# Kernel optimization log

Measured on AMD Instinct MI355X. Metric: run time of the kernel, lower is better.

## Reference

```python
import jax, jax.numpy as jnp
import numpy as np

B, L, D = 2, 4096, 2048
H = 8
DK = D // H   # head qk dim = 256
DV = D // H   # head v dim = 256
KCONV = 4
BT = 64       # chunk size
EPS = 1e-5


def setup_inputs() -> dict:
    key = jax.random.key(0)
    ks = jax.random.split(key, 10)
    s = 0.02  # xavier-ish init scale (gain 2**-2.5)
    return {
        "hidden_states": jax.random.normal(ks[0], (B, L, D), jnp.float32),
        "Wq": jax.random.normal(ks[1], (D, D), jnp.float32) * s,
        "Wk": jax.random.normal(ks[2], (D, D), jnp.float32) * s,
        "Wv": jax.random.normal(ks[3], (D, D), jnp.float32) * s,
        "Wb": jax.random.normal(ks[4], (H, D), jnp.float32) * s,
        "conv_q": jax.random.normal(ks[5], (D, KCONV), jnp.float32) * 0.5,
        "conv_k": jax.random.normal(ks[6], (D, KCONV), jnp.float32) * 0.5,
        "conv_v": jax.random.normal(ks[7], (D, KCONV), jnp.float32) * 0.5,
        "g_norm": jnp.ones((DV,), jnp.float32),
        "Wo": jax.random.normal(ks[8], (D, D), jnp.float32) * s,
    }


def _causal_conv_silu(x, w):
    # depthwise causal conv1d (ShortConvolution), x: [B,L,C], w: [C,K]; silu activation
    K = w.shape[1]
    xp = jnp.pad(x, ((0, 0), (K - 1, 0), (0, 0)))
    Lx = x.shape[1]
    y = xp[:, 0:Lx, :] * w[:, 0]
    for j in range(1, K):
        y = y + xp[:, j:j + Lx, :] * w[:, j]
    return jax.nn.silu(y)


def _l2norm(x):
    return x * jax.lax.rsqrt(jnp.sum(x * x, -1, keepdims=True) + 1e-6)


def _chunk_delta_rule(q, k, v, beta):
    # q,k: [B,H,L,DK], v: [B,H,L,DV], beta: [B,H,L]
    b, h, Lq, dk = q.shape
    dv = v.shape[-1]
    nc = Lq // BT
    q = q * (dk ** -0.5)
    kb = k * beta[..., None]
    vb = v * beta[..., None]
    ch = lambda x: x.reshape(b, h, nc, BT, x.shape[-1])
    qc, kc, kbc, vbc = ch(q), ch(k), ch(kb), ch(vb)
    tri_s = jnp.tril(jnp.ones((BT, BT), bool), -1)  # strictly lower
    tri = jnp.tril(jnp.ones((BT, BT), bool))        # lower incl diag
    # M = strict_lower(K_beta K^T); T = (I+M)^{-1} via unit-lower triangular solve
    M = jnp.where(tri_s, jnp.einsum('bhntd,bhnsd->bhnts', kbc, kc), 0.0)
    Lmat = jnp.eye(BT, dtype=q.dtype) + M
    W = jax.scipy.linalg.solve_triangular(Lmat, kbc, lower=True, unit_diagonal=True)  # T @ k_beta
    U = jax.scipy.linalg.solve_triangular(Lmat, vbc, lower=True, unit_diagonal=True)  # T @ v_beta

    def step(S, xs):
        q_i, k_i, w_i, u_i = xs  # each [b,h,BT,d]
        attn = jnp.where(tri, jnp.einsum('bhtd,bhsd->bhts', q_i, k_i), 0.0)
        u_new = u_i - jnp.einsum('bhtd,bhdv->bhtv', w_i, S)
        o_i = jnp.einsum('bhtd,bhdv->bhtv', q_i, S) + jnp.einsum('bhts,bhsv->bhtv', attn, u_new)
        S = S + jnp.einsum('bhtd,bhtv->bhdv', k_i, u_new)
        return S, o_i

    mv = lambda x: jnp.moveaxis(x, 2, 0)  # chunk axis to front for scan
    S0 = jnp.zeros((b, h, dk, dv), q.dtype)
    S, o = jax.lax.scan(step, S0, (mv(qc), mv(kc), mv(W), mv(U)))
    o = jnp.moveaxis(o, 0, 2).reshape(b, h, Lq, dv)
    return o, S


def reference(hidden_states, Wq, Wk, Wv, Wb, conv_q, conv_k, conv_v, g_norm, Wo):
    hs = hidden_states
    q = _causal_conv_silu(hs @ Wq.T, conv_q)
    k = _causal_conv_silu(hs @ Wk.T, conv_k)
    v = _causal_conv_silu(hs @ Wv.T, conv_v)
    tohead = lambda x: x.reshape(B, L, H, -1).transpose(0, 2, 1, 3)  # b l (h d) -> b h l d
    q, k, v = tohead(q), tohead(k), tohead(v)
    q, k = _l2norm(q), _l2norm(k)
    beta = jax.nn.sigmoid(hs @ Wb.T).transpose(0, 2, 1)  # [B,H,L]
    o, _ = _chunk_delta_rule(q, k, v, beta)
    o = o.transpose(0, 2, 1, 3)  # [B,L,H,DV]
    o = o * jax.lax.rsqrt(jnp.mean(o * o, -1, keepdims=True) + EPS) * g_norm  # per-head RMSNorm
    return o.reshape(B, L, D) @ Wo.T
```

## Files before the change

### kernel.cpp

```cpp
#include <hip/hip_runtime.h>
#include <stdint.h>

#define TOK    8192
#define LDIM   4096
#define DDIM   2048
#define NBH    16
#define DK     256
#define NCHUNK 64

typedef __attribute__((ext_vector_type(8))) short bf16x8;
typedef __attribute__((ext_vector_type(4))) float f32x4;

#define MFMA(a,b,c) __builtin_amdgcn_mfma_f32_16x16x32_bf16((a),(b),(c),0,0,0)

__device__ __forceinline__ unsigned short f2bf(float f){
  union { float f; uint32_t u; } v; v.f = f;
  uint32_t r = v.u + 0x7FFFu + ((v.u >> 16) & 1u);
  return (unsigned short)(r >> 16);
}
__device__ __forceinline__ float bf2f(unsigned short u){
  union { uint32_t u; float f; } v; v.u = ((uint32_t)u) << 16;
  return v.f;
}

typedef __attribute__((address_space(1))) unsigned int as1_u32;
typedef __attribute__((address_space(3))) unsigned int as3_u32;
__device__ __forceinline__ void gload16(const void* g, void* l){
  __builtin_amdgcn_global_load_lds((const as1_u32*)g, (as3_u32*)l, 16, 0, 0);
}

__global__ void k_guard(float* o){ if (threadIdx.x == 0) o[0] = 0.f; }

__global__ __launch_bounds__(256) void k_f2bf(const float* __restrict__ s,
                                              unsigned short* __restrict__ d, int n)
{
  int i = (blockIdx.x*256 + threadIdx.x)*4;
  if (i >= n) return;
  float4 v = *(const float4*)(s + i);
  ushort4 o; o.x=f2bf(v.x); o.y=f2bf(v.y); o.z=f2bf(v.z); o.w=f2bf(v.w);
  *(ushort4*)(d + i) = o;
}

__global__ __launch_bounds__(256) void k_beta(const float* __restrict__ hs,
                                              const float* __restrict__ Wb,
                                              float* __restrict__ beta)
{
  const long t = blockIdx.x;
  const int tid = threadIdx.x;
  float acc[8] = {0,0,0,0,0,0,0,0};
  const float* xr = hs + t*DDIM;
  for (int i = tid; i < DDIM; i += 256){
    float x = xr[i];
    #pragma unroll
    for (int h=0; h<8; h++) acc[h] += x * Wb[h*DDIM + i];
  }
  __shared__ float red[8][4];
  const int w = tid >> 6, lane = tid & 63;
  #pragma unroll
  for (int h=0; h<8; h++){
    float s = acc[h];
    #pragma unroll
    for (int off=32; off; off>>=1) s += __shfl_down(s, off, 64);
    if (lane == 0) red[h][w] = s;
  }
  __syncthreads();
  if (tid < 8){
    float s = red[tid][0]+red[tid][1]+red[tid][2]+red[tid][3];
    float bv = 1.f/(1.f + __expf(-s));
    int b = (int)(t >> 12), l = (int)(t & 4095);
    beta[((long)(b*8 + tid))*LDIM + l] = bv;
  }
}

template <bool F32OUT>
__global__ __launch_bounds__(256,2) void k_gemm_bt(
    const unsigned short* __restrict__ A, const unsigned short* __restrict__ Bw,
    void* __restrict__ Cv, int M, int N, int K)
{
  __shared__ unsigned short As[128*32];
  __shared__ unsigned short Bs[128*32];
  const int tid = threadIdx.x;
  const int w = tid >> 6, l = tid & 63;
  const int lo = l & 15, quad = l >> 4;
  const int wm = w >> 1, wn = w & 1;
  const int gx = gridDim.x;
  int id = blockIdx.y * gx + blockIdx.x;
  const int nwg = gx * gridDim.y;
  if ((nwg & 7) == 0){
    const int q8 = nwg >> 3;
    id = (id & 7) * q8 + (id >> 3);
  }
  const int bx = id % gx, by = id / gx;
  const long tm = (long)by * 128, tn = (long)bx * 128;
  const int slot0 = (w*2+0)*64 + l;
  const int slot1 = (w*2+1)*64 + l;
  const int r0 = slot0 >> 2, c0 = (slot0 & 3) * 8;
  const int r1 = slot1 >> 2, c1 = (slot1 & 3) * 8;
  const unsigned short* pA0 = A  + (tm + r0)*(long)K + c0;
  const unsigned short* pA1 = A  + (tm + r1)*(long)K + c1;
  const unsigned short* pB0 = Bw + (tn + r0)*(long)K + c0;
  const unsigned short* pB1 = Bw + (tn + r1)*(long)K + c1;
  unsigned short* lA0 = &As[slot0*8]; unsigned short* lA1 = &As[slot1*8];
  unsigned short* lB0 = &Bs[slot0*8]; unsigned short* lB1 = &Bs[slot1*8];
  f32x4 acc[4][4] = {};
  for (int k0 = 0; k0 < K; k0 += 32){
    __syncthreads();
    gload16(pA0 + k0, lA0);
    gload16(pA1 + k0, lA1);
    gload16(pB0 + k0, lB0);
    gload16(pB1 + k0, lB1);
    __syncthreads();
    bf16x8 af[4], bg[4];
    #pragma unroll
    for (int i=0;i<4;i++){
      af[i] = *(const bf16x8*)&As[(wm*64 + i*16 + lo)*32 + quad*8];
      bg[i] = *(const bf16x8*)&Bs[(wn*64 + i*16 + lo)*32 + quad*8];
    }
    #pragma unroll
    for (int mt=0; mt<4; mt++)
      #pragma unroll
      for (int nt=0; nt<4; nt++)
        acc[mt][nt] = MFMA(af[mt], bg[nt], acc[mt][nt]);
  }
  #pragma unroll
  for (int mt=0; mt<4; mt++)
    #pragma unroll
    for (int nt=0; nt<4; nt++)
      #pragma unroll
      for (int r=0; r<4; r++){
        long m = tm + wm*64 + mt*16 + quad*4 + r;
        long n = tn + wn*64 + nt*16 + lo;
        if (F32OUT) ((float*)Cv)[m*N + n] = acc[mt][nt][r];
        else ((unsigned short*)Cv)[m*N + n] = f2bf(acc[mt][nt][r]);
      }
}

__global__ __launch_bounds__(256) void k_conv(
  const unsigned short* __restrict__ X, const float* __restrict__ Wc,
  const float* __restrict__ beta,
  unsigned short* __restrict__ O, int mode)
{
  const int lt = blockIdx.x, bh = blockIdx.y;
  const int b = bh >> 3, h = bh & 7;
  const int d = threadIdx.x;
  const int ch = h*256 + d;
  const int l0 = lt*64;
  const unsigned short* xp = X + (long)b*LDIM*DDIM + ch;
  const float4 wv = *(const float4*)(Wc + ch*4);
  float x0=0.f, x1=0.f, x2=0.f;
  if (l0 >= 3){
    x0 = bf2f(xp[(long)(l0-3)*DDIM]);
    x1 = bf2f(xp[(long)(l0-2)*DDIM]);
    x2 = bf2f(xp[(long)(l0-1)*DDIM]);
  }
  float y[64];
  #pragma unroll
  for (int i=0;i<64;i++){
    float x3 = bf2f(xp[(long)(l0+i)*DDIM]);
    float s = x0*wv.x + x1*wv.y + x2*wv.z + x3*wv.w;
    y[i] = s / (1.f + __expf(-s));
    x0 = x1; x1 = x2; x2 = x3;
  }
  unsigned short* op = O + (long)bh*LDIM*DK + d;
  if (mode == 2){
    const float* bet = beta + (long)bh*LDIM + l0;
    #pragma unroll
    for (int i=0;i<64;i++) op[(long)(l0+i)*DK] = f2bf(y[i]*bet[i]);
    return;
  }
  __shared__ float red[64*4];
  __shared__ float scl[64];
  const int wv_i = threadIdx.x >> 6, lane = threadIdx.x & 63;
  #pragma unroll
  for (int i=0;i<64;i++){
    float ss = y[i]*y[i];
    #pragma unroll
    for (int off=32; off; off>>=1) ss += __shfl_down(ss, off, 64);
    if (lane == 0) red[i*4 + wv_i] = ss;
  }
  __syncthreads();
  if (threadIdx.x < 64){
    int i = threadIdx.x;
    float s = red[i*4]+red[i*4+1]+red[i*4+2]+red[i*4+3];
    scl[i] = rsqrtf(s + 1e-6f) * (mode==0 ? 0.0625f : 1.f);
  }
  __syncthreads();
  #pragma unroll
  for (int i=0;i<64;i++) op[(long)(l0+i)*DK] = f2bf(y[i]*scl[i]);
}

__global__ __launch_bounds__(256) void k_transpose(
  const unsigned short* __restrict__ kH, unsigned short* __restrict__ kT)
{
  const int lt = blockIdx.x, dt = blockIdx.y, bh = blockIdx.z;
  __shared__ unsigned short tk[64][72];
  const int tid = threadIdx.x;
  const int rl = tid >> 2, c0 = (tid & 3) * 16;
  const long base = ((long)bh*LDIM + lt*64 + rl)*DK + dt*64 + c0;
  *(bf16x8*)&tk[rl][c0]   = *(const bf16x8*)(kH + base);
  *(bf16x8*)&tk[rl][c0+8] = *(const bf16x8*)(kH + base + 8);
  __syncthreads();
  const int rd = tid >> 2, lc0 = (tid & 3) * 16;
  bf16x8 ok0, ok1;
  #pragma unroll
  for (int j=0;j<16;j++){
    unsigned short kraw = tk[lc0+j][rd];
    if (j < 8) ok0[j] = (short)kraw; else ok1[j-8] = (short)kraw;
  }
  const long ob = (((long)bh*NCHUNK + lt)*DK + dt*64 + rd)*64 + lc0;
  *(bf16x8*)(kT + ob) = ok0; *(bf16x8*)(kT + ob + 8) = ok1;
}

__global__ __launch_bounds__(256) void k_passA(
  const unsigned short* __restrict__ qH, const unsigned short* __restrict__ kH,
  const unsigned short* vbH,
  const unsigned short* __restrict__ kT,
  const float* __restrict__ beta,
  unsigned short* Wout,
  unsigned short* __restrict__ Uout,
  unsigned short* __restrict__ Aout)
{
  const int c = blockIdx.x, bh = blockIdx.y;
  __shared__ unsigned short Nn[64*72];
  __shared__ unsigned short NT[64*72];
  __shared__ unsigned short Pb[64*72];
  __shared__ unsigned short vT[256*72];
  const int tid = threadIdx.x;
  const int w = tid >> 6, l = tid & 63, lo = l & 15, quad = l >> 4;
  const long tokBase = (long)bh*LDIM + c*64;
  const unsigned short* qrow = qH + tokBase*DK;
  const unsigned short* krow = kH + tokBase*DK;
  const float bv = beta[tokBase + w*16 + lo];

  {
    const int r = tid >> 2, cs = (tid & 3) * 64;
    const unsigned short* vrow = vbH + (tokBase + r)*DK + cs;
    bf16x8 vv[8];
    #pragma unroll
    for (int j=0;j<8;j++) vv[j] = *(const bf16x8*)(vrow + j*8);
    #pragma unroll
    for (int j=0;j<8;j++)
      #pragma unroll
      for (int e=0;e<8;e++)
        vT[(cs + j*8 + e)*72 + r] = (unsigned short)vv[j][e];
  }

  f32x4 mAcc[4] = {}; f32x4 aAcc[4] = {};
  #pragma unroll
  for (int ks=0; ks<8; ks++){
    bf16x8 kf[4];
    #pragma unroll
    for (int nt=0; nt<4; nt++)
      kf[nt] = *(const bf16x8*)&krow[(nt*16+lo)*DK + ks*32 + quad*8];
    bf16x8 qf  = *(const bf16x8*)&qrow[(w*16+lo)*DK + ks*32 + quad*8];
    bf16x8 kfw = *(const bf16x8*)&krow[(w*16+lo)*DK + ks*32 + quad*8];
    bf16x8 kbf;
    #pragma unroll
    for (int j=0;j<8;j++) kbf[j] = (short)f2bf(bf2f((unsigned short)kfw[j]) * bv);
    #pragma unroll
    for (int nt=0; nt<4; nt++){
      mAcc[nt] = MFMA(kbf, kf[nt], mAcc[nt]);
      aAcc[nt] = MFMA(qf,  kf[nt], aAcc[nt]);
    }
  }
  unsigned short* Ap = Aout + ((long)bh*NCHUNK + c)*64*64;
  #pragma unroll
  for (int nt=0; nt<4; nt++)
    #pragma unroll
    for (int r=0; r<4; r++){
      int t = w*16 + quad*4 + r, s = nt*16 + lo;
      float mv = (t > s) ? mAcc[nt][r] : 0.f;
      unsigned short mb = f2bf(mv);
      Nn[t*72+s] = mb;
      NT[s*72+t] = mb;
      Pb[t*72+s] = f2bf((t==s ? 1.f : 0.f) - mv);
      Ap[t*64+s] = f2bf((t >= s) ? aAcc[nt][r] : 0.f);
    }
  __syncthreads();

  #pragma unroll 1
  for (int it=0; it<5; it++){
    bf16x8 aN[2], aP[2], bN[2][4];
    #pragma unroll
    for (int ks=0; ks<2; ks++){
      aN[ks] = *(const bf16x8*)&Nn[(w*16+lo)*72 + ks*32 + quad*8];
      aP[ks] = *(const bf16x8*)&Pb[(w*16+lo)*72 + ks*32 + quad*8];
      #pragma unroll
      for (int nt=0; nt<4; nt++)
        bN[ks][nt] = *(const bf16x8*)&NT[(nt*16+lo)*72 + ks*32 + quad*8];
    }
    f32x4 pp[4];
    #pragma unroll
    for (int nt=0; nt<4; nt++)
      #pragma unroll
      for (int r=0; r<4; r++)
        pp[nt][r] = bf2f(Pb[(w*16+quad*4+r)*72 + nt*16+lo]);
    __syncthreads();
    f32x4 sq[4] = {};
    #pragma unroll
    for (int ks=0; ks<2; ks++)
      #pragma unroll
      for (int nt=0; nt<4; nt++)
        sq[nt] = MFMA(aN[ks], bN[ks][nt], sq[nt]);
    #pragma unroll
    for (int nt=0; nt<4; nt++)
      #pragma unroll
      for (int r=0; r<4; r++){
        int t = w*16 + quad*4 + r, s = nt*16 + lo;
        unsigned short vb2 = f2bf(sq[nt][r]);
        Nn[t*72+s] = vb2; NT[s*72+t] = vb2;
      }
    __syncthreads();
    #pragma unroll
    for (int ks=0; ks<2; ks++)
      #pragma unroll
      for (int nt=0; nt<4; nt++){
        bf16x8 b = *(const bf16x8*)&NT[(nt*16+lo)*72 + ks*32 + quad*8];
        pp[nt] = MFMA(aP[ks], b, pp[nt]);
      }
    #pragma unroll
    for (int nt=0; nt<4; nt++)
      #pragma unroll
      for (int r=0; r<4; r++)
        Pb[(w*16+quad*4+r)*72 + nt*16+lo] = f2bf(pp[nt][r]);
    __syncthreads();
  }

  float b8[2][8];
  #pragma unroll
  for (int ks=0; ks<2; ks++)
    #pragma unroll
    for (int e=0; e<8; e++)
      b8[ks][e] = beta[tokBase + ks*32 + quad*8 + e];
  const unsigned short* kTb = kT + ((long)bh*NCHUNK + c)*DK*64;
  unsigned short* Wp = Wout + tokBase*DK;
  unsigned short* Up = Uout + tokBase*DK;
  #pragma unroll 1
  for (int nl=0; nl<4; nl++){
    const int d = (w*4 + nl)*16 + lo;
    f32x4 wa[4] = {}; f32x4 ua[4] = {};
    #pragma unroll
    for (int ks=0; ks<2; ks++){
      bf16x8 braw = *(const bf16x8*)&kTb[(long)d*64 + ks*32 + quad*8];
      bf16x8 bw;
      #pragma unroll
      for (int e=0; e<8; e++) bw[e] = (short)f2bf(bf2f((unsigned short)braw[e]) * b8[ks][e]);
      bf16x8 bu = *(const bf16x8*)&vT[d*72 + ks*32 + quad*8];
      #pragma unroll
      for (int mt=0; mt<4; mt++){
        bf16x8 a = *(const bf16x8*)&Pb[(mt*16+lo)*72 + ks*32 + quad*8];
        wa[mt] = MFMA(a, bw, wa[mt]);
        ua[mt] = MFMA(a, bu, ua[mt]);
      }
    }
    #pragma unroll
    for (int mt=0; mt<4; mt++)
      #pragma unroll
      for (int r=0; r<4; r++){
        int t = mt*16 + quad*4 + r;
        Wp[t*DK + d] = f2bf(wa[mt][r]);
        Up[t*DK + d] = f2bf(ua[mt][r]);
      }
  }
}

__device__ __forceinline__ int sidx(int n, int d){
  return n*256 + (((d>>3) ^ (n&7))<<3) + (d&7);
}
__device__ __forceinline__ int uidx(int n, int t){
  return n*64 + ((((t>>3) ^ (n&7)) & 7)<<3) + (t&7);
}

struct PrefWU {
  bf16x8 wf[8];
  unsigned short uf[8];
};

__device__ __forceinline__ void load_wu(PrefWU& P,
    const unsigned short* __restrict__ Wp, const unsigned short* __restrict__ Up,
    int c, int w, int lo, int quad, int vb)
{
  const unsigned short* Wc = Wp + (long)c*64*DK;
  const unsigned short* Uc = Up + (long)c*64*DK;
  #pragma unroll
  for (int ks=0; ks<8; ks++)
    P.wf[ks] = *(const bf16x8*)&Wc[(w*16+lo)*DK + ks*32 + quad*8];
  const int t0 = w*16 + quad*4;
  #pragma unroll
  for (int nt=0; nt<2; nt++)
    #pragma unroll
    for (int r=0; r<4; r++)
      P.uf[nt*4+r] = Uc[(t0+r)*DK + vb*32 + nt*16 + lo];
}

__device__ __forceinline__ void scan_chunk(const PrefWU& P, int c,
  const unsigned short* __restrict__ qp, const unsigned short* __restrict__ kTp,
  const unsigned short* __restrict__ Ap, unsigned short* __restrict__ op,
  const unsigned short* __restrict__ Srd, unsigned short* __restrict__ Swr,
  unsigned short* __restrict__ u_l, f32x4 (&S)[4][2],
  int w, int lo, int quad, int vb)
{
  const unsigned short* qc = qp + (long)c*64*DK;
  const unsigned short* Ac = Ap + (long)c*64*64;
  const unsigned short* kc = kTp + (long)c*DK*64;
  bf16x8 qf[8], af[2], kf[4][2];
  #pragma unroll
  for (int ks=0; ks<8; ks++)
    qf[ks] = *(const bf16x8*)&qc[(w*16+lo)*DK + ks*32 + quad*8];
  #pragma unroll
  for (int ks=0; ks<2; ks++)
    af[ks] = *(const bf16x8*)&Ac[(w*16+lo)*64 + ks*32 + quad*8];
  #pragma unroll
  for (int mtl=0; mtl<4; mtl++)
    #pragma unroll
    for (int ks=0; ks<2; ks++)
      kf[mtl][ks] = *(const bf16x8*)&kc[(w*64+mtl*16+lo)*64 + ks*32 + quad*8];

  f32x4 ua[2] = {}; f32x4 oa[2] = {};
  #pragma unroll
  for (int ks=0; ks<8; ks++)
    #pragma unroll
    for (int nt=0; nt<2; nt++){
      bf16x8 b = *(const bf16x8*)&Srd[sidx(nt*16+lo, ks*32+quad*8)];
      ua[nt] = MFMA(P.wf[ks], b, ua[nt]);
      oa[nt] = MFMA(qf[ks],  b, oa[nt]);
    }
  {
    const int t0 = w*16 + quad*4;
    #pragma unroll
    for (int nt=0; nt<2; nt++){
      const int n = nt*16 + lo;
      ushort4 pk;
      pk.x = f2bf(bf2f(P.uf[nt*4+0]) - ua[nt][0]);
      pk.y = f2bf(bf2f(P.uf[nt*4+1]) - ua[nt][1]);
      pk.z = f2bf(bf2f(P.uf[nt*4+2]) - ua[nt][2]);
      pk.w = f2bf(bf2f(P.uf[nt*4+3]) - ua[nt][3]);
      *(ushort4*)&u_l[uidx(n, t0)] = pk;
    }
  }
  __syncthreads();
  #pragma unroll
  for (int ks=0; ks<2; ks++)
    #pragma unroll
    for (int nt=0; nt<2; nt++){
      bf16x8 b = *(const bf16x8*)&u_l[uidx(nt*16+lo, ks*32+quad*8)];
      oa[nt] = MFMA(af[ks], b, oa[nt]);
    }
  #pragma unroll
  for (int nt=0; nt<2; nt++)
    #pragma unroll
    for (int r=0; r<4; r++)
      op[(long)(c*64 + w*16 + quad*4 + r)*DK + vb*32 + nt*16 + lo] = f2bf(oa[nt][r]);
  #pragma unroll
  for (int mtl=0; mtl<4; mtl++)
    #pragma unroll
    for (int ks=0; ks<2; ks++)
      #pragma unroll
      for (int nt=0; nt<2; nt++){
        bf16x8 b = *(const bf16x8*)&u_l[uidx(nt*16+lo, ks*32+quad*8)];
        S[mtl][nt] = MFMA(kf[mtl][ks], b, S[mtl][nt]);
      }
  #pragma unroll
  for (int mtl=0; mtl<4; mtl++)
    #pragma unroll
    for (int nt=0; nt<2; nt++){
      const int n = nt*16 + lo;
      const int d0 = w*64 + mtl*16 + quad*4;
      ushort4 pk;
      pk.x = f2bf(S[mtl][nt][0]); pk.y = f2bf(S[mtl][nt][1]);
      pk.z = f2bf(S[mtl][nt][2]); pk.w = f2bf(S[mtl][nt][3]);
      *(ushort4*)&Swr[sidx(n, d0)] = pk;
    }
  __syncthreads();
}

__global__ __launch_bounds__(256,1) void k_scan(
  const unsigned short* __restrict__ Wm, const unsigned short* __restrict__ Um,
  const unsigned short* __restrict__ qH, const unsigned short* __restrict__ kT,
  const unsigned short* __restrict__ Abuf, unsigned short* __restrict__ oH)
{
  const int bh = blockIdx.x, vb = blockIdx.y;
  __shared__ unsigned short S_l[2][32*256];
  __shared__ unsigned short u_l[32*64];
  const int tid = threadIdx.x;
  const int w = tid >> 6, l = tid & 63, lo = l & 15, quad = l >> 4;
  for (int i = tid; i < 2048; i += 256) ((unsigned long long*)S_l[0])[i] = 0ULL;
  f32x4 S[4][2] = {};
  const long hb = (long)bh * LDIM;
  const unsigned short* Wp = Wm + hb*DK;
  const unsigned short* Up = Um + hb*DK;
  const unsigned short* qp = qH + hb*DK;
  const unsigned short* kTp = kT + (long)bh*NCHUNK*DK*64;
  const unsigned short* Ap = Abuf + (long)bh*NCHUNK*64*64;
  unsigned short* op = oH + hb*DK;
  PrefWU PA, PB;
  load_wu(PA, Wp, Up, 0, w, lo, quad, vb);
  __syncthreads();
  #pragma unroll 1
  for (int c = 0; c < NCHUNK; c += 2){
    load_wu(PB, Wp, Up, c+1, w, lo, quad, vb);
    scan_chunk(PA, c,   qp, kTp, Ap, op, S_l[0], S_l[1], u_l, S, w, lo, quad, vb);
    load_wu(PA, Wp, Up, (c+2 < NCHUNK) ? c+2 : NCHUNK-1, w, lo, quad, vb);
    scan_chunk(PB, c+1, qp, kTp, Ap, op, S_l[1], S_l[0], u_l, S, w, lo, quad, vb);
  }
}

__global__ __launch_bounds__(64) void k_rms(
  const unsigned short* __restrict__ oH, const float* __restrict__ g,
  unsigned short* __restrict__ oN)
{
  const int ln = blockIdx.x, bh = blockIdx.y;
  const int b = bh >> 3, h = bh & 7;
  ushort4 u = *(const ushort4*)(oH + ((long)bh*LDIM + ln)*DK + threadIdx.x*4);
  float4 v; v.x = bf2f(u.x); v.y = bf2f(u.y); v.z = bf2f(u.z); v.w = bf2f(u.w);
  float ss = v.x*v.x + v.y*v.y + v.z*v.z + v.w*v.w;
  #pragma unroll
  for (int off=32; off; off>>=1) ss += __shfl_down(ss, off, 64);
  ss = __shfl(ss, 0, 64);
  const float sc = rsqrtf(ss*(1.f/DK) + 1e-5f);
  const float4 gv = *(const float4*)(g + threadIdx.x*4);
  unsigned short* o = oN + ((long)b*LDIM + ln)*DDIM + h*DK + threadIdx.x*4;
  ushort4 pk; pk.x=f2bf(v.x*sc*gv.x); pk.y=f2bf(v.y*sc*gv.y);
  pk.z=f2bf(v.z*sc*gv.z); pk.w=f2bf(v.w*sc*gv.w);
  *(ushort4*)o = pk;
}

extern "C" void kernel_launch(void* const* d_in, const int* in_sizes, int n_in,
                              void* d_out, int out_size, void* d_ws, size_t ws_size,
                              hipStream_t stream)
{
  (void)in_sizes; (void)n_in; (void)out_size;
  const float* hs = (const float*)d_in[0];
  const float* Wq = (const float*)d_in[1];
  const float* Wk = (const float*)d_in[2];
  const float* Wv = (const float*)d_in[3];
  const float* Wb = (const float*)d_in[4];
  const float* cq = (const float*)d_in[5];
  const float* ck = (const float*)d_in[6];
  const float* cv = (const float*)d_in[7];
  const float* gn = (const float*)d_in[8];
  const float* Wo = (const float*)d_in[9];

  const size_t SZ_TD2 = (size_t)TOK*DDIM*2;
  const size_t SZ_DD2 = (size_t)DDIM*DDIM*2;
  const size_t NEED  = 5*SZ_TD2 + 2*SZ_DD2 + (size_t)NBH*LDIM*4;
  const size_t NEEDW = NEED + SZ_TD2;
  if (ws_size < NEED){ k_guard<<<1, 64, 0, stream>>>((float*)d_out); return; }

  char* p = (char*)d_ws;
  unsigned short* bufA = (unsigned short*)p;      p += SZ_TD2;
  unsigned short* bufB = (unsigned short*)p;      p += SZ_DD2;
  unsigned short* bufC = (unsigned short*)p;      p += SZ_TD2;
  unsigned short* bufD = (unsigned short*)p;      p += SZ_TD2;
  unsigned short* bufE = (unsigned short*)p;      p += SZ_TD2;
  unsigned short* bufF = (unsigned short*)p;      p += SZ_TD2;
  unsigned short* bufG = (unsigned short*)p;      p += SZ_DD2;
  float*          beta = (float*)p;               p += (size_t)NBH*LDIM*4;
  unsigned short* bufW = (ws_size >= NEEDW) ? (unsigned short*)p : bufF;

  const dim3 gg(DDIM/128, TOK/128);
  const dim3 cg(LDIM/64, NBH);
  const int nTD = TOK*DDIM, nDD = DDIM*DDIM;

  k_f2bf<<<dim3(nTD/1024), 256, 0, stream>>>(hs, bufA, nTD);
  k_beta<<<dim3(TOK), 256, 0, stream>>>(hs, Wb, beta);

  k_f2bf<<<dim3(nDD/1024), 256, 0, stream>>>(Wq, bufB, nDD);
  k_gemm_bt<false><<<gg, 256, 0, stream>>>(bufA, bufB, bufC, TOK, DDIM, DDIM);
  k_conv<<<cg, 256, 0, stream>>>(bufC, cq, beta, bufD, 0);

  k_f2bf<<<dim3(nDD/1024), 256, 0, stream>>>(Wk, bufB, nDD);
  k_gemm_bt<false><<<gg, 256, 0, stream>>>(bufA, bufB, bufC, TOK, DDIM, DDIM);
  k_conv<<<cg, 256, 0, stream>>>(bufC, ck, beta, bufE, 1);

  k_f2bf<<<dim3(nDD/1024), 256, 0, stream>>>(Wv, bufB, nDD);
  k_gemm_bt<false><<<gg, 256, 0, stream>>>(bufA, bufB, bufC, TOK, DDIM, DDIM);
  k_conv<<<cg, 256, 0, stream>>>(bufC, cv, beta, bufF, 2);

  k_transpose<<<dim3(LDIM/64, DK/64, NBH), 256, 0, stream>>>(bufE, bufC);
  k_passA<<<dim3(NCHUNK, NBH), 256, 0, stream>>>(bufD, bufE, bufF, bufC, beta,
                                                 bufW, bufA , bufG);
  k_scan<<<dim3(NBH, 8), 256, 0, stream>>>(bufW, bufA, bufD, bufC, bufG, bufE);
  k_rms<<<dim3(LDIM, NBH), 64, 0, stream>>>(bufE, gn, bufC);

  k_f2bf<<<dim3(nDD/1024), 256, 0, stream>>>(Wo, bufB, nDD);
  k_gemm_bt<true><<<gg, 256, 0, stream>>>(bufC, bufB, d_out , TOK, DDIM, DDIM);
}
```

Baseline: 945.6 us.

## Split scan value dimension into 16-wide slices and single-buffer W/U prefetch

```diff
diff --git a/kernel.cpp b/kernel.cpp
--- a/kernel.cpp
+++ b/kernel.cpp
@@ -7,6 +7,7 @@
 #define NBH    16
 #define DK     256
 #define NCHUNK 64
+#define DVS    16
 
 typedef __attribute__((ext_vector_type(8))) short bf16x8;
 typedef __attribute__((ext_vector_type(4))) float f32x4;
@@ -373,7 +374,7 @@
 
 struct PrefWU {
   bf16x8 wf[8];
-  unsigned short uf[8];
+  unsigned short uf[4];
 };
 
 __device__ __forceinline__ void load_wu(PrefWU& P,
@@ -387,90 +388,88 @@
     P.wf[ks] = *(const bf16x8*)&Wc[(w*16+lo)*DK + ks*32 + quad*8];
   const int t0 = w*16 + quad*4;
   #pragma unroll
-  for (int nt=0; nt<2; nt++)
-    #pragma unroll
-    for (int r=0; r<4; r++)
-      P.uf[nt*4+r] = Uc[(t0+r)*DK + vb*32 + nt*16 + lo];
-}
-
-__device__ __forceinline__ void scan_chunk(const PrefWU& P, int c,
+  for (int r=0; r<4; r++)
+    P.uf[r] = Uc[(t0+r)*DK + vb*DVS + lo];
+}
+
+__device__ __forceinline__ void scan_chunk(PrefWU& P, int c, int cnext,
+  const unsigned short* __restrict__ Wp, const unsigned short* __restrict__ Up,
   const unsigned short* __restrict__ qp, const unsigned short* __restrict__ kTp,
   const unsigned short* __restrict__ Ap, unsigned short* __restrict__ op,
   const unsigned short* __restrict__ Srd, unsigned short* __restrict__ Swr,
-  unsigned short* __restrict__ u_l, f32x4 (&S)[4][2],
+  unsigned short* __restrict__ u_l, f32x4 (&S)[4],
   int w, int lo, int quad, int vb)
 {
   const unsigned short* qc = qp + (long)c*64*DK;
   const unsigned short* Ac = Ap + (long)c*64*64;
   const unsigned short* kc = kTp + (long)c*DK*64;
-  bf16x8 qf[8], af[2], kf[4][2];
+  const int t0 = w*16 + quad*4;
+  bf16x8 qf[8], af[2];
   #pragma unroll
   for (int ks=0; ks<8; ks++)
     qf[ks] = *(const bf16x8*)&qc[(w*16+lo)*DK + ks*32 + quad*8];
   #pragma unroll
   for (int ks=0; ks<2; ks++)
     af[ks] = *(const bf16x8*)&Ac[(w*16+lo)*64 + ks*32 + quad*8];
+
+  bf16x8 sb[8];
+  #pragma unroll
+  for (int ks=0; ks<8; ks++)
+    sb[ks] = *(const bf16x8*)&Srd[sidx(lo, ks*32+quad*8)];
+  f32x4 ua0 = {}, ua1 = {};
+  #pragma unroll
+  for (int ks=0; ks<4; ks++){
+    ua0 = MFMA(P.wf[ks],   sb[ks],   ua0);
+    ua1 = MFMA(P.wf[ks+4], sb[ks+4], ua1);
+  }
+  {
+    ushort4 pk;
+    pk.x = f2bf(bf2f(P.uf[0]) - (ua0[0]+ua1[0]));
+    pk.y = f2bf(bf2f(P.uf[1]) - (ua0[1]+ua1[1]));
+    pk.z = f2bf(bf2f(P.uf[2]) - (ua0[2]+ua1[2]));
+    pk.w = f2bf(bf2f(P.uf[3]) - (ua0[3]+ua1[3]));
+    *(ushort4*)&u_l[uidx(lo, t0)] = pk;
+  }
+  __syncthreads();
+
+  load_wu(P, Wp, Up, cnext, w, lo, quad, vb);
+  bf16x8 kf[4][2];
   #pragma unroll
   for (int mtl=0; mtl<4; mtl++)
     #pragma unroll
     for (int ks=0; ks<2; ks++)
       kf[mtl][ks] = *(const bf16x8*)&kc[(w*64+mtl*16+lo)*64 + ks*32 + quad*8];
 
-  f32x4 ua[2] = {}; f32x4 oa[2] = {};
-  #pragma unroll
-  for (int ks=0; ks<8; ks++)
-    #pragma unroll
-    for (int nt=0; nt<2; nt++){
-      bf16x8 b = *(const bf16x8*)&Srd[sidx(nt*16+lo, ks*32+quad*8)];
-      ua[nt] = MFMA(P.wf[ks], b, ua[nt]);
-      oa[nt] = MFMA(qf[ks],  b, oa[nt]);
-    }
-  {
-    const int t0 = w*16 + quad*4;
-    #pragma unroll
-    for (int nt=0; nt<2; nt++){
-      const int n = nt*16 + lo;
-      ushort4 pk;
-      pk.x = f2bf(bf2f(P.uf[nt*4+0]) - ua[nt][0]);
-      pk.y = f2bf(bf2f(P.uf[nt*4+1]) - ua[nt][1]);
-      pk.z = f2bf(bf2f(P.uf[nt*4+2]) - ua[nt][2]);
-      pk.w = f2bf(bf2f(P.uf[nt*4+3]) - ua[nt][3]);
-      *(ushort4*)&u_l[uidx(n, t0)] = pk;
-    }
-  }
-  __syncthreads();
+  f32x4 oa0 = {}, oa1 = {};
+  #pragma unroll
+  for (int ks=0; ks<4; ks++){
+    oa0 = MFMA(qf[ks],   sb[ks],   oa0);
+    oa1 = MFMA(qf[ks+4], sb[ks+4], oa1);
+  }
+  bf16x8 ub[2];
   #pragma unroll
   for (int ks=0; ks<2; ks++)
-    #pragma unroll
-    for (int nt=0; nt<2; nt++){
-      bf16x8 b = *(const bf16x8*)&u_l[uidx(nt*16+lo, ks*32+quad*8)];
-      oa[nt] = MFMA(af[ks], b, oa[nt]);
-    }
-  #pragma unroll
-  for (int nt=0; nt<2; nt++)
-    #pragma unroll
-    for (int r=0; r<4; r++)
-      op[(long)(c*64 + w*16 + quad*4 + r)*DK + vb*32 + nt*16 + lo] = f2bf(oa[nt][r]);
+    ub[ks] = *(const bf16x8*)&u_l[uidx(lo, ks*32+quad*8)];
+  #pragma unroll
+  for (int ks=0; ks<2; ks++)
+    oa0 = MFMA(af[ks], ub[ks], oa0);
+  #pragma unroll
+  for (int r=0; r<4; r++)
+    op[(long)(c*64 + t0 + r)*DK + vb*DVS + lo] = f2bf(oa0[r] + oa1[r]);
+
   #pragma unroll
   for (int mtl=0; mtl<4; mtl++)
     #pragma unroll
     for (int ks=0; ks<2; ks++)
-      #pragma unroll
-      for (int nt=0; nt<2; nt++){
-        bf16x8 b = *(const bf16x8*)&u_l[uidx(nt*16+lo, ks*32+quad*8)];
-        S[mtl][nt] = MFMA(kf[mtl][ks], b, S[mtl][nt]);
-      }
-  #pragma unroll
-  for (int mtl=0; mtl<4; mtl++)
-    #pragma unroll
-    for (int nt=0; nt<2; nt++){
-      const int n = nt*16 + lo;
-      const int d0 = w*64 + mtl*16 + quad*4;
-      ushort4 pk;
-      pk.x = f2bf(S[mtl][nt][0]); pk.y = f2bf(S[mtl][nt][1]);
-      pk.z = f2bf(S[mtl][nt][2]); pk.w = f2bf(S[mtl][nt][3]);
-      *(ushort4*)&Swr[sidx(n, d0)] = pk;
-    }
+      S[mtl] = MFMA(kf[mtl][ks], ub[ks], S[mtl]);
+  #pragma unroll
+  for (int mtl=0; mtl<4; mtl++){
+    const int d0 = w*64 + mtl*16 + quad*4;
+    ushort4 pk;
+    pk.x = f2bf(S[mtl][0]); pk.y = f2bf(S[mtl][1]);
+    pk.z = f2bf(S[mtl][2]); pk.w = f2bf(S[mtl][3]);
+    *(ushort4*)&Swr[sidx(lo, d0)] = pk;
+  }
   __syncthreads();
 }
 
@@ -480,12 +479,12 @@
   const unsigned short* __restrict__ Abuf, unsigned short* __restrict__ oH)
 {
   const int bh = blockIdx.x, vb = blockIdx.y;
-  __shared__ unsigned short S_l[2][32*256];
-  __shared__ unsigned short u_l[32*64];
+  __shared__ unsigned short S_l[2][DVS*256];
+  __shared__ unsigned short u_l[DVS*64];
   const int tid = threadIdx.x;
   const int w = tid >> 6, l = tid & 63, lo = l & 15, quad = l >> 4;
-  for (int i = tid; i < 2048; i += 256) ((unsigned long long*)S_l[0])[i] = 0ULL;
-  f32x4 S[4][2] = {};
+  for (int i = tid; i < DVS*256/4; i += 256) ((unsigned long long*)S_l[0])[i] = 0ULL;
+  f32x4 S[4] = {};
   const long hb = (long)bh * LDIM;
   const unsigned short* Wp = Wm + hb*DK;
   const unsigned short* Up = Um + hb*DK;
@@ -493,15 +492,14 @@
   const unsigned short* kTp = kT + (long)bh*NCHUNK*DK*64;
   const unsigned short* Ap = Abuf + (long)bh*NCHUNK*64*64;
   unsigned short* op = oH + hb*DK;
-  PrefWU PA, PB;
-  load_wu(PA, Wp, Up, 0, w, lo, quad, vb);
+  PrefWU P;
+  load_wu(P, Wp, Up, 0, w, lo, quad, vb);
   __syncthreads();
   #pragma unroll 1
   for (int c = 0; c < NCHUNK; c += 2){
-    load_wu(PB, Wp, Up, c+1, w, lo, quad, vb);
-    scan_chunk(PA, c,   qp, kTp, Ap, op, S_l[0], S_l[1], u_l, S, w, lo, quad, vb);
-    load_wu(PA, Wp, Up, (c+2 < NCHUNK) ? c+2 : NCHUNK-1, w, lo, quad, vb);
-    scan_chunk(PB, c+1, qp, kTp, Ap, op, S_l[1], S_l[0], u_l, S, w, lo, quad, vb);
+    scan_chunk(P, c,   c+1, Wp, Up, qp, kTp, Ap, op, S_l[0], S_l[1], u_l, S, w, lo, quad, vb);
+    scan_chunk(P, c+1, (c+2 < NCHUNK) ? c+2 : NCHUNK-1,
+               Wp, Up, qp, kTp, Ap, op, S_l[1], S_l[0], u_l, S, w, lo, quad, vb);
   }
 }
 
@@ -580,7 +578,7 @@
   k_transpose<<<dim3(LDIM/64, DK/64, NBH), 256, 0, stream>>>(bufE, bufC);
   k_passA<<<dim3(NCHUNK, NBH), 256, 0, stream>>>(bufD, bufE, bufF, bufC, beta,
                                                  bufW, bufA , bufG);
-  k_scan<<<dim3(NBH, 8), 256, 0, stream>>>(bufW, bufA, bufD, bufC, bufG, bufE);
+  k_scan<<<dim3(NBH, 16), 256, 0, stream>>>(bufW, bufA, bufD, bufC, bufG, bufE);
   k_rms<<<dim3(LDIM, NBH), 64, 0, stream>>>(bufE, gn, bufC);
 
   k_f2bf<<<dim3(nDD/1024), 256, 0, stream>>>(Wo, bufB, nDD);
```

Result: faster. 912.6 us (-3.5%).
